# Performance work log

Hardware: AMD Instinct MI355X
Metric: run time of the kernel (lower is better)

## Reference

```python
import jax, jax.numpy as jnp
import numpy as np

HEADS = 8
HEAD_DIM = 64
SCALE = (2 * HEAD_DIM) ** -0.5


def setup_inputs() -> dict:
    key = jax.random.key(0)
    k1, k2, k3, k4, k5 = jax.random.split(key, 5)
    B, N, D = 2, 2048, 512
    inner = HEADS * HEAD_DIM  # 512
    return {
        "x1": jax.random.normal(k1, (B, N, D), dtype=jnp.float32),
        "x2": jax.random.normal(k2, (B, N, D), dtype=jnp.float32),
        "W_qkv1": jax.random.normal(k3, (D, 3 * inner), dtype=jnp.float32) * 0.02,
        "W_qkv2": jax.random.normal(k4, (D, 3 * inner), dtype=jnp.float32) * 0.02,
        "W_out": jax.random.normal(k5, (inner, D), dtype=jnp.float32) * 0.02,
        "b_out": jnp.zeros((D,), dtype=jnp.float32),
    }


def _split_heads(t):
    # [b, n, h*d] -> [b, h, n, d]
    b, n, hd = t.shape
    return t.reshape(b, n, HEADS, HEAD_DIM).transpose(0, 2, 1, 3)


def reference(x1, x2, W_qkv1, W_qkv2, W_out, b_out):
    qkv1 = x1 @ W_qkv1  # [b, n, 3*inner]
    qkv2 = x2 @ W_qkv2
    q1, k1, v1 = (_split_heads(t) for t in jnp.split(qkv1, 3, axis=-1))
    q2, k2, v2 = (_split_heads(t) for t in jnp.split(qkv2, 3, axis=-1))

    # fused dual-stream logits: scale * (q1 k1^T + q2 k2^T)  [b, h, n, n]
    dots = SCALE * (jnp.einsum("bhnd,bhmd->bhnm", q1, k1)
                    + jnp.einsum("bhnd,bhmd->bhnm", q2, k2))
    attn = jax.nn.softmax(dots, axis=-1)

    out1 = jnp.einsum("bhnm,bhmd->bhnd", attn, v1)
    out2 = jnp.einsum("bhnm,bhmd->bhnd", attn, v2)

    def _merge(t):
        b, h, n, d = t.shape
        return t.transpose(0, 2, 1, 3).reshape(b, n, h * d)

    out = jnp.concatenate([_merge(out1), _merge(out2)], axis=1)  # [b, 2n, inner]
    return out @ W_out + b_out
```

## Files before the change

### kernel.cpp

```cpp
#include <hip/hip_runtime.h>
#include <hip/hip_bf16.h>

typedef __attribute__((ext_vector_type(8))) short bf16x8;
typedef __attribute__((ext_vector_type(4))) float f32x4;
typedef __attribute__((ext_vector_type(16))) float f32x16;
typedef __attribute__((ext_vector_type(4))) short s16x4;
typedef __attribute__((ext_vector_type(4))) int i32x4;

#define MFMA(a, b, c) __builtin_amdgcn_mfma_f32_16x16x32_bf16(a, b, c, 0, 0, 0)
#define MFMA32(a, b, c) __builtin_amdgcn_mfma_f32_32x32x16_bf16(a, b, c, 0, 0, 0)

#define SCALE_F 0.08838834764831845f

__device__ __forceinline__ short f2bf(float f) {
  __hip_bfloat16 h = __float2bfloat16(f);
  return *reinterpret_cast<short*>(&h);
}

__device__ __forceinline__ void gld_lds16(const void* g, void* s) {
  __builtin_amdgcn_global_load_lds(
      (const __attribute__((address_space(1))) void*)g,
      (__attribute__((address_space(3))) void*)s, 16, 0, 0);
}

__global__ void cast_bf16_dual(const float* __restrict__ a,
                               const float* __restrict__ b,
                               short* __restrict__ oa, short* __restrict__ ob,
                               int n) {
  int idx = (blockIdx.x * 256 + threadIdx.x) * 4;
  const float* src = a;
  short* dst = oa;
  if (idx >= n) { idx -= n; src = b; dst = ob; }
  float4 v = *(const float4*)&src[idx];
  s16x4 o;
  o.x = f2bf(v.x); o.y = f2bf(v.y); o.z = f2bf(v.z); o.w = f2bf(v.w);
  *(s16x4*)&dst[idx] = o;
}

__global__ __launch_bounds__(256) void cast_transpose_tiled(
    const float* __restrict__ Wq1, const float* __restrict__ Wq2,
    const float* __restrict__ Wo, short* __restrict__ W1t,
    short* __restrict__ W2t, short* __restrict__ Wot) {
  __shared__ float t[64][65];
  int bid = blockIdx.x;
  const float* src;
  short* dst;
  int C, r0, c0;
  bool isq;
  if (bid < 384) {
    src = (bid < 192) ? Wq1 : Wq2;
    dst = (bid < 192) ? W1t : W2t;
    int tb = bid % 192;
    C = 1536; isq = true;
    r0 = (tb / 24) * 64; c0 = (tb % 24) * 64;
  } else {
    src = Wo; dst = Wot;
    int tb = bid - 384;
    C = 512; isq = false;
    r0 = (tb / 8) * 64; c0 = (tb % 8) * 64;
  }
  const int tid = threadIdx.x;
  const int lr = tid >> 4, lc = (tid & 15) * 4;
#pragma unroll
  for (int i = 0; i < 4; ++i) {
    float4 v = *(const float4*)&src[(size_t)(r0 + lr + 16 * i) * C + c0 + lc];
    t[lr + 16 * i][lc + 0] = v.x;
    t[lr + 16 * i][lc + 1] = v.y;
    t[lr + 16 * i][lc + 2] = v.z;
    t[lr + 16 * i][lc + 3] = v.w;
  }
  __syncthreads();
  const int oc = tid >> 2, orr = (tid & 3) * 16;
  const float sc = (isq && (c0 + oc) < 512) ? SCALE_F : 1.0f;
  short* dbase = dst + (size_t)(c0 + oc) * 512 + r0 + orr;
#pragma unroll
  for (int jj = 0; jj < 4; ++jj) {
    s16x4 ov;
    ov.x = f2bf(t[orr + 4 * jj + 0][oc] * sc);
    ov.y = f2bf(t[orr + 4 * jj + 1][oc] * sc);
    ov.z = f2bf(t[orr + 4 * jj + 2][oc] * sc);
    ov.w = f2bf(t[orr + 4 * jj + 3][oc] * sc);
    *(s16x4*)&dbase[4 * jj] = ov;
  }
}

__global__ __launch_bounds__(256) void gemm_qkv(
    const short* __restrict__ xb1, const short* __restrict__ xb2,
    const short* __restrict__ W1t, const short* __restrict__ W2t,
    short* __restrict__ QK1, short* __restrict__ QK2,
    short* __restrict__ Vt1, short* __restrict__ Vt2) {
  __shared__ short As[128 * 64];
  __shared__ short Bs[128 * 64];
  const int tid = threadIdx.x;
  const int w = tid >> 6, l = tid & 63;
  const int sid = blockIdx.y >= 12;
  const short* A = sid ? xb2 : xb1;
  const short* Bt = sid ? W2t : W1t;
  short* C0 = sid ? QK2 : QK1;
  short* C1 = sid ? Vt2 : Vt1;
  const int m0 = blockIdx.x * 128;
  const int n0 = (sid ? blockIdx.y - 12 : blockIdx.y) * 128;
  const int mi = (w >> 1) * 64, ni = (w & 1) * 64;
  const int lrow = l & 15, lk8 = (l >> 4) * 8;
  const int K = 512;

  f32x4 acc[4][4] = {};

  for (int k0 = 0; k0 < K; k0 += 64) {
    for (int g = 0; g < 4; ++g) {
      int c = g * 256 + w * 64 + l;
      int row = c >> 3, c8 = (c & 7) * 8;
      int ldsoff = (g * 256 + w * 64) * 8;
      gld_lds16(A + (size_t)(m0 + row) * K + k0 + c8, (void*)(As + ldsoff));
      gld_lds16(Bt + (size_t)(n0 + row) * K + k0 + c8, (void*)(Bs + ldsoff));
    }
    __syncthreads();
    __builtin_amdgcn_s_setprio(1);
    for (int kp = 0; kp < 2; ++kp) {
      bf16x8 af[4], bfr[4];
      for (int mf = 0; mf < 4; ++mf)
        af[mf] = *(const bf16x8*)&As[(mi + mf * 16 + lrow) * 64 + kp * 32 + lk8];
      for (int nf = 0; nf < 4; ++nf)
        bfr[nf] = *(const bf16x8*)&Bs[(ni + nf * 16 + lrow) * 64 + kp * 32 + lk8];
      for (int mf = 0; mf < 4; ++mf)
        for (int nf = 0; nf < 4; ++nf)
          acc[mf][nf] = MFMA(af[mf], bfr[nf], acc[mf][nf]);
    }
    __builtin_amdgcn_s_setprio(0);
    __syncthreads();
  }

  for (int mf = 0; mf < 4; ++mf)
    for (int nf = 0; nf < 4; ++nf)
      for (int r = 0; r < 4; ++r) {
        int row = m0 + mi + mf * 16 + (l >> 4) * 4 + r;
        int col = n0 + ni + nf * 16 + lrow;
        float v = acc[mf][nf][r];
        if (col < 1024) {
          C0[(size_t)row * 1024 + col] = f2bf(v);
        } else {
          int b = row >> 11, n = row & 2047;
          int cv = col - 1024, h = cv >> 6, d = cv & 63;
          C1[(((size_t)(b * 8 + h) * 64 + d) << 11) + n] = f2bf(v);
        }
      }
}

__global__ __launch_bounds__(256) void gemm_out(const short* __restrict__ A,
                                                const short* __restrict__ Bt,
                                                float* __restrict__ Cf,
                                                const float* __restrict__ bias) {
  __shared__ short As[64 * 64];
  __shared__ short Bs[128 * 64];
  const int tid = threadIdx.x;
  const int w = tid >> 6, l = tid & 63;
  const int m0 = blockIdx.x * 64, n0 = blockIdx.y * 128;
  const int mi = (w >> 1) * 32, ni = (w & 1) * 64;
  const int lrow = l & 15, lk8 = (l >> 4) * 8;
  const int K = 512, N = 512;

  f32x4 acc[2][4] = {};

  for (int k0 = 0; k0 < K; k0 += 64) {
    for (int g = 0; g < 2; ++g) {
      int c = g * 256 + tid;
      int row = c >> 3, c8 = (c & 7) * 8;
      gld_lds16(A + (size_t)(m0 + row) * K + k0 + c8, (void*)(As + c * 8));
    }
    for (int g = 0; g < 4; ++g) {
      int c = g * 256 + tid;
      int row = c >> 3, c8 = (c & 7) * 8;
      gld_lds16(Bt + (size_t)(n0 + row) * K + k0 + c8, (void*)(Bs + c * 8));
    }
    __syncthreads();
    __builtin_amdgcn_s_setprio(1);
    for (int kp = 0; kp < 2; ++kp) {
      bf16x8 af[2], bfr[4];
      for (int mf = 0; mf < 2; ++mf)
        af[mf] = *(const bf16x8*)&As[(mi + mf * 16 + lrow) * 64 + kp * 32 + lk8];
      for (int nf = 0; nf < 4; ++nf)
        bfr[nf] = *(const bf16x8*)&Bs[(ni + nf * 16 + lrow) * 64 + kp * 32 + lk8];
      for (int mf = 0; mf < 2; ++mf)
        for (int nf = 0; nf < 4; ++nf)
          acc[mf][nf] = MFMA(af[mf], bfr[nf], acc[mf][nf]);
    }
    __builtin_amdgcn_s_setprio(0);
    __syncthreads();
  }

  for (int mf = 0; mf < 2; ++mf)
    for (int nf = 0; nf < 4; ++nf)
      for (int r = 0; r < 4; ++r) {
        int row = m0 + mi + mf * 16 + (l >> 4) * 4 + r;
        int col = n0 + ni + nf * 16 + lrow;
        Cf[(size_t)row * N + col] = acc[mf][nf][r] + bias[col];
      }
}

__global__ __launch_bounds__(256, 2) void attn_kernel(
    const short* __restrict__ QK1, const short* __restrict__ QK2,
    const short* __restrict__ Vt1, const short* __restrict__ Vt2,
    short* __restrict__ Ocat) {
  __shared__ short lds[32768];
  short* K1s = lds;
  short* K2s = lds + 8192;
  short* V1s = lds + 16384;
  short* V2s = lds + 24576;

  const int tid = threadIdx.x;
  const int w = tid >> 6, l = tid & 63;
  const int wq = w & 1, wk = w >> 1;
  const int lq = l & 31, hi = l >> 5;
  const int qb = blockIdx.x, bh = blockIdx.y;
  const int b = bh >> 3, h = bh & 7;

  const short* Q1p = QK1 + (size_t)b * 2048 * 1024 + h * 64;
  const short* K1p = Q1p + 512;
  const short* Q2p = QK2 + (size_t)b * 2048 * 1024 + h * 64;
  const short* K2p = Q2p + 512;
  const short* V1p = Vt1 + (size_t)bh * 64 * 2048;
  const short* V2p = Vt2 + (size_t)bh * 64 * 2048;

  const int qrow = qb * 64 + wq * 32 + lq;
  bf16x8 q1f[4], q2f[4];
#pragma unroll
  for (int ck = 0; ck < 4; ++ck) {
    q1f[ck] = *(const bf16x8*)&Q1p[(size_t)qrow * 1024 + ck * 16 + hi * 8];
    q2f[ck] = *(const bf16x8*)&Q2p[(size_t)qrow * 1024 + ck * 16 + hi * 8];
  }

  f32x16 o1a = {}, o1b = {}, o2a = {}, o2b = {};
  float mrun = -1e30f, lrun = 0.f;

  auto stage_K = [&](int buf, int kt) {
    const int kv0 = kt * 64;
#pragma unroll
    for (int gg = 0; gg < 2; ++gg) {
      int cl = gg * 256 + tid;
      int row = cl >> 3;
      int lc = (cl & 7) ^ (row & 7);
      int lr = row & 31;
      int krow = kv0 + ((row >> 5) << 5) + (((lr >> 3) & 1) << 4) +
                 (((lr >> 2) & 1) << 3) + (((lr >> 4) & 1) << 2) + (lr & 3);
      int doff = buf * 4096 + cl * 8;
      gld_lds16(K1p + (size_t)krow * 1024 + lc * 8, (void*)(K1s + doff));
      gld_lds16(K2p + (size_t)krow * 1024 + lc * 8, (void*)(K2s + doff));
    }
  };
  auto stage_V = [&](int buf, int kt) {
    const int kv0 = kt * 64;
#pragma unroll
    for (int gg = 0; gg < 2; ++gg) {
      int cl = gg * 256 + tid;
      int row = cl >> 3;
      int lc = (cl & 7) ^ (row & 7);
      int doff = buf * 4096 + cl * 8;
      gld_lds16(V1p + (size_t)row * 2048 + kv0 + lc * 8, (void*)(V1s + doff));
      gld_lds16(V2p + (size_t)row * 2048 + kv0 + lc * 8, (void*)(V2s + doff));
    }
  };
  auto swo = [&](int row, int kc) { return row * 64 + ((kc ^ (row & 7)) * 8); };

  auto qk_tile = [&](int buf) -> f32x16 {
    const int krd = 32 * wk + lq;
    f32x16 s = {};
    __builtin_amdgcn_s_setprio(1);
#pragma unroll
    for (int ck = 0; ck < 4; ++ck) {
      bf16x8 k1 = *(const bf16x8*)&K1s[buf * 4096 + swo(krd, 2 * ck + hi)];
      bf16x8 k2 = *(const bf16x8*)&K2s[buf * 4096 + swo(krd, 2 * ck + hi)];
      s = MFMA32(k1, q1f[ck], s);
      s = MFMA32(k2, q2f[ck], s);
    }
    __builtin_amdgcn_s_setprio(0);
    return s;
  };

  auto smpv = [&](int buf, f32x16 s) {
    float mx = s[0];
#pragma unroll
    for (int i = 1; i < 16; ++i) mx = fmaxf(mx, s[i]);
    if (!__all(mx - mrun <= 8.0f)) {
      float rm = fmaxf(mx, __shfl_xor(mx, 32));
      float newm = fmaxf(mrun, rm);
      float corr = __expf(mrun - newm);
      mrun = newm;
      lrun *= corr;
#pragma unroll
      for (int i = 0; i < 16; ++i) {
        o1a[i] *= corr; o1b[i] *= corr; o2a[i] *= corr; o2b[i] *= corr;
      }
    }
    float p[16];
#pragma unroll
    for (int i = 0; i < 16; ++i) { p[i] = __expf(s[i] - mrun); lrun += p[i]; }

    __hip_bfloat162 a0 = __float22bfloat162_rn(float2{p[0], p[1]});
    __hip_bfloat162 a1 = __float22bfloat162_rn(float2{p[2], p[3]});
    __hip_bfloat162 a2 = __float22bfloat162_rn(float2{p[8], p[9]});
    __hip_bfloat162 a3 = __float22bfloat162_rn(float2{p[10], p[11]});
    __hip_bfloat162 b0 = __float22bfloat162_rn(float2{p[4], p[5]});
    __hip_bfloat162 b1 = __float22bfloat162_rn(float2{p[6], p[7]});
    __hip_bfloat162 b2 = __float22bfloat162_rn(float2{p[12], p[13]});
    __hip_bfloat162 b3 = __float22bfloat162_rn(float2{p[14], p[15]});
    i32x4 w0 = {*(int*)&a0, *(int*)&a1, *(int*)&a2, *(int*)&a3};
    i32x4 w1 = {*(int*)&b0, *(int*)&b1, *(int*)&b2, *(int*)&b3};
    bf16x8 pb0 = *(bf16x8*)&w0, pb1 = *(bf16x8*)&w1;

    __builtin_amdgcn_s_setprio(1);
#pragma unroll
    for (int c = 0; c < 2; ++c) {
      bf16x8 pb = c ? pb1 : pb0;
      int kcv = 4 * wk + 2 * c + hi;
      bf16x8 v1a = *(const bf16x8*)&V1s[buf * 4096 + swo(lq, kcv)];
      bf16x8 v1b = *(const bf16x8*)&V1s[buf * 4096 + swo(32 + lq, kcv)];
      bf16x8 v2a = *(const bf16x8*)&V2s[buf * 4096 + swo(lq, kcv)];
      bf16x8 v2b = *(const bf16x8*)&V2s[buf * 4096 + swo(32 + lq, kcv)];
      o1a = MFMA32(v1a, pb, o1a);
      o1b = MFMA32(v1b, pb, o1b);
      o2a = MFMA32(v2a, pb, o2a);
      o2b = MFMA32(v2b, pb, o2b);
    }
    __builtin_amdgcn_s_setprio(0);
  };

  stage_K(0, 0);
  stage_V(0, 0);
  stage_K(1, 1);
  asm volatile("s_waitcnt vmcnt(4)" ::: "memory");
  __builtin_amdgcn_s_barrier();
  f32x16 sprev = qk_tile(0);
  stage_V(1, 1);

  int cur = 0;
  for (int t = 0; t < 31; ++t) {
    asm volatile("s_waitcnt vmcnt(4) lgkmcnt(0)" ::: "memory");
    __builtin_amdgcn_s_barrier();
    if (t < 30) stage_K(cur, t + 2);
    f32x16 snew = qk_tile(cur ^ 1);
    smpv(cur, sprev);
    asm volatile("s_waitcnt lgkmcnt(0)" ::: "memory");
    __builtin_amdgcn_s_barrier();
    if (t < 30) stage_V(cur, t + 2);
    sprev = snew;
    cur ^= 1;
  }
  asm volatile("s_waitcnt vmcnt(0)" ::: "memory");
  __builtin_amdgcn_s_barrier();
  smpv(cur, sprev);

  lrun += __shfl_xor(lrun, 32);
  float* cb = (float*)lds;
  float* rg = cb + wq * 4224;
  if (wk == 1) {
#pragma unroll
    for (int i = 0; i < 16; ++i) {
      rg[i * 64 + l] = o1a[i];
      rg[(16 + i) * 64 + l] = o1b[i];
      rg[(32 + i) * 64 + l] = o2a[i];
      rg[(48 + i) * 64 + l] = o2b[i];
    }
    rg[4096 + l] = mrun;
    rg[4160 + l] = lrun;
  }
  __syncthreads();
  if (wk == 0) {
    float m1 = rg[4096 + l], l1 = rg[4160 + l];
    float mstar = fmaxf(mrun, m1);
    float e0 = __expf(mrun - mstar), e1 = __expf(m1 - mstar);
    float inv = 1.0f / (lrun * e0 + l1 * e1);
    float av0 = e0 * inv, av1 = e1 * inv;
#pragma unroll
    for (int i = 0; i < 16; ++i) {
      o1a[i] = o1a[i] * av0 + rg[i * 64 + l] * av1;
      o1b[i] = o1b[i] * av0 + rg[(16 + i) * 64 + l] * av1;
      o2a[i] = o2a[i] * av0 + rg[(32 + i) * 64 + l] * av1;
      o2b[i] = o2b[i] * av0 + rg[(48 + i) * 64 + l] * av1;
    }
    const size_t base1 = ((size_t)b * 4096 + qrow) * 512 + h * 64;
    const size_t base2 = base1 + (size_t)2048 * 512;
#pragma unroll
    for (int rq = 0; rq < 4; ++rq) {
      int d0 = 8 * rq + 4 * hi;
      s16x4 ov;
      ov.x = f2bf(o1a[rq * 4 + 0]); ov.y = f2bf(o1a[rq * 4 + 1]);
      ov.z = f2bf(o1a[rq * 4 + 2]); ov.w = f2bf(o1a[rq * 4 + 3]);
      *(s16x4*)&Ocat[base1 + d0] = ov;
      ov.x = f2bf(o1b[rq * 4 + 0]); ov.y = f2bf(o1b[rq * 4 + 1]);
      ov.z = f2bf(o1b[rq * 4 + 2]); ov.w = f2bf(o1b[rq * 4 + 3]);
      *(s16x4*)&Ocat[base1 + 32 + d0] = ov;
      ov.x = f2bf(o2a[rq * 4 + 0]); ov.y = f2bf(o2a[rq * 4 + 1]);
      ov.z = f2bf(o2a[rq * 4 + 2]); ov.w = f2bf(o2a[rq * 4 + 3]);
      *(s16x4*)&Ocat[base2 + d0] = ov;
      ov.x = f2bf(o2b[rq * 4 + 0]); ov.y = f2bf(o2b[rq * 4 + 1]);
      ov.z = f2bf(o2b[rq * 4 + 2]); ov.w = f2bf(o2b[rq * 4 + 3]);
      *(s16x4*)&Ocat[base2 + 32 + d0] = ov;
    }
  }
}

extern "C" void kernel_launch(void* const* d_in, const int* in_sizes, int n_in,
                              void* d_out, int out_size, void* d_ws,
                              size_t ws_size, hipStream_t stream) {
  const float* x1 = (const float*)d_in[0];
  const float* x2 = (const float*)d_in[1];
  const float* Wq1 = (const float*)d_in[2];
  const float* Wq2 = (const float*)d_in[3];
  const float* Wo = (const float*)d_in[4];
  const float* bo = (const float*)d_in[5];
  float* out = (float*)d_out;

  short* p = (short*)d_ws;
  short* xb1 = p;  p += (size_t)4096 * 512;
  short* xb2 = p;  p += (size_t)4096 * 512;
  short* W1t = p;  p += (size_t)1536 * 512;
  short* W2t = p;  p += (size_t)1536 * 512;
  short* Wot = p;  p += (size_t)512 * 512;
  short* QK1 = p;  p += (size_t)4096 * 1024;
  short* QK2 = p;  p += (size_t)4096 * 1024;
  short* Vt1 = p;  p += (size_t)2 * 8 * 64 * 2048;
  short* Vt2 = p;  p += (size_t)2 * 8 * 64 * 2048;
  short* Ocat = p; p += (size_t)8192 * 512;

  cast_bf16_dual<<<4096, 256, 0, stream>>>(x1, x2, xb1, xb2, 4096 * 512);
  cast_transpose_tiled<<<448, 256, 0, stream>>>(Wq1, Wq2, Wo, W1t, W2t, Wot);

  gemm_qkv<<<dim3(32, 24), 256, 0, stream>>>(xb1, xb2, W1t, W2t, QK1, QK2,
                                             Vt1, Vt2);

  attn_kernel<<<dim3(32, 16), 256, 0, stream>>>(QK1, QK2, Vt1, Vt2, Ocat);

  gemm_out<<<dim3(128, 4), 256, 0, stream>>>(Ocat, Wot, out, bo);
}
```

Baseline: 102.3 us.

## Merge cast kernels, use exp2 softmax, simplify attention pipeline to single-stage prefetch

Merges the input-cast and weight cast-transpose kernels into one launch to save a kernel launch. Folds log2(e) into the Q scaling so softmax uses exp2 directly, removing a multiply per exponential. Replaces the software-pipelined attention loop (QK of the next tile overlapped with softmax/PV of the previous, K and V staged separately) with a simpler double-buffered loop that prefetches K and V together for the next tile. The simpler schedule loses the cross-tile overlap of the QK MFMAs with the softmax work.

```diff
diff --git a/kernel.cpp b/kernel.cpp
--- a/kernel.cpp
+++ b/kernel.cpp
@@ -11,6 +11,9 @@
 #define MFMA32(a, b, c) __builtin_amdgcn_mfma_f32_32x32x16_bf16(a, b, c, 0, 0, 0)
 
 #define SCALE_F 0.08838834764831845f
+#define LOG2E_F 1.4426950408889634f
+#define THR2 11.541560327111708f
+#define EXP2(x) __builtin_exp2f(x)
 
 __device__ __forceinline__ short f2bf(float f) {
   __hip_bfloat16 h = __float2bfloat16(f);
@@ -23,26 +26,27 @@
       (__attribute__((address_space(3))) void*)s, 16, 0, 0);
 }
 
-__global__ void cast_bf16_dual(const float* __restrict__ a,
-                               const float* __restrict__ b,
-                               short* __restrict__ oa, short* __restrict__ ob,
-                               int n) {
-  int idx = (blockIdx.x * 256 + threadIdx.x) * 4;
-  const float* src = a;
-  short* dst = oa;
-  if (idx >= n) { idx -= n; src = b; dst = ob; }
-  float4 v = *(const float4*)&src[idx];
-  s16x4 o;
-  o.x = f2bf(v.x); o.y = f2bf(v.y); o.z = f2bf(v.z); o.w = f2bf(v.w);
-  *(s16x4*)&dst[idx] = o;
-}
-
-__global__ __launch_bounds__(256) void cast_transpose_tiled(
+__global__ __launch_bounds__(256) void preprocess(
+    const float* __restrict__ x1, const float* __restrict__ x2,
     const float* __restrict__ Wq1, const float* __restrict__ Wq2,
-    const float* __restrict__ Wo, short* __restrict__ W1t,
-    short* __restrict__ W2t, short* __restrict__ Wot) {
+    const float* __restrict__ Wo, short* __restrict__ xb1,
+    short* __restrict__ xb2, short* __restrict__ W1t, short* __restrict__ W2t,
+    short* __restrict__ Wot) {
   __shared__ float t[64][65];
+  const int tid = threadIdx.x;
   int bid = blockIdx.x;
+  if (bid < 4096) {
+    int idx = (bid * 256 + tid) * 4;
+    const float* src = x1;
+    short* dst = xb1;
+    if (idx >= 4096 * 512) { idx -= 4096 * 512; src = x2; dst = xb2; }
+    float4 v = *(const float4*)&src[idx];
+    s16x4 o;
+    o.x = f2bf(v.x); o.y = f2bf(v.y); o.z = f2bf(v.z); o.w = f2bf(v.w);
+    *(s16x4*)&dst[idx] = o;
+    return;
+  }
+  bid -= 4096;
   const float* src;
   short* dst;
   int C, r0, c0;
@@ -59,7 +63,6 @@
     C = 512; isq = false;
     r0 = (tb / 8) * 64; c0 = (tb % 8) * 64;
   }
-  const int tid = threadIdx.x;
   const int lr = tid >> 4, lc = (tid & 15) * 4;
 #pragma unroll
   for (int i = 0; i < 4; ++i) {
@@ -71,7 +74,8 @@
   }
   __syncthreads();
   const int oc = tid >> 2, orr = (tid & 3) * 16;
-  const float sc = (isq && (c0 + oc) < 512) ? SCALE_F : 1.0f;
+  const float sc =
+      (isq && (c0 + oc) < 512) ? SCALE_F * LOG2E_F : 1.0f;
   short* dbase = dst + (size_t)(c0 + oc) * 512 + r0 + orr;
 #pragma unroll
   for (int jj = 0; jj < 4; ++jj) {
@@ -232,7 +236,7 @@
   f32x16 o1a = {}, o1b = {}, o2a = {}, o2b = {};
   float mrun = -1e30f, lrun = 0.f;
 
-  auto stage_K = [&](int buf, int kt) {
+  auto stage = [&](int buf, int kt) {
     const int kv0 = kt * 64;
 #pragma unroll
     for (int gg = 0; gg < 2; ++gg) {
@@ -245,45 +249,43 @@
       int doff = buf * 4096 + cl * 8;
       gld_lds16(K1p + (size_t)krow * 1024 + lc * 8, (void*)(K1s + doff));
       gld_lds16(K2p + (size_t)krow * 1024 + lc * 8, (void*)(K2s + doff));
-    }
-  };
-  auto stage_V = [&](int buf, int kt) {
-    const int kv0 = kt * 64;
-#pragma unroll
-    for (int gg = 0; gg < 2; ++gg) {
-      int cl = gg * 256 + tid;
-      int row = cl >> 3;
-      int lc = (cl & 7) ^ (row & 7);
-      int doff = buf * 4096 + cl * 8;
       gld_lds16(V1p + (size_t)row * 2048 + kv0 + lc * 8, (void*)(V1s + doff));
       gld_lds16(V2p + (size_t)row * 2048 + kv0 + lc * 8, (void*)(V2s + doff));
     }
   };
   auto swo = [&](int row, int kc) { return row * 64 + ((kc ^ (row & 7)) * 8); };
 
-  auto qk_tile = [&](int buf) -> f32x16 {
+  int cur = 0;
+  stage(0, 0);
+
+  for (int kt = 0; kt < 32; ++kt) {
+    if (kt + 1 < 32) {
+      stage(cur ^ 1, kt + 1);
+      asm volatile("s_waitcnt vmcnt(8)" ::: "memory");
+    } else {
+      asm volatile("s_waitcnt vmcnt(0)" ::: "memory");
+    }
+    __builtin_amdgcn_s_barrier();
+
     const int krd = 32 * wk + lq;
     f32x16 s = {};
     __builtin_amdgcn_s_setprio(1);
 #pragma unroll
     for (int ck = 0; ck < 4; ++ck) {
-      bf16x8 k1 = *(const bf16x8*)&K1s[buf * 4096 + swo(krd, 2 * ck + hi)];
-      bf16x8 k2 = *(const bf16x8*)&K2s[buf * 4096 + swo(krd, 2 * ck + hi)];
+      bf16x8 k1 = *(const bf16x8*)&K1s[cur * 4096 + swo(krd, 2 * ck + hi)];
+      bf16x8 k2 = *(const bf16x8*)&K2s[cur * 4096 + swo(krd, 2 * ck + hi)];
       s = MFMA32(k1, q1f[ck], s);
       s = MFMA32(k2, q2f[ck], s);
     }
     __builtin_amdgcn_s_setprio(0);
-    return s;
-  };
-
-  auto smpv = [&](int buf, f32x16 s) {
+
     float mx = s[0];
 #pragma unroll
     for (int i = 1; i < 16; ++i) mx = fmaxf(mx, s[i]);
-    if (!__all(mx - mrun <= 8.0f)) {
+    if (!__all(mx - mrun <= THR2)) {
       float rm = fmaxf(mx, __shfl_xor(mx, 32));
       float newm = fmaxf(mrun, rm);
-      float corr = __expf(mrun - newm);
+      float corr = EXP2(mrun - newm);
       mrun = newm;
       lrun *= corr;
 #pragma unroll
@@ -293,7 +295,7 @@
     }
     float p[16];
 #pragma unroll
-    for (int i = 0; i < 16; ++i) { p[i] = __expf(s[i] - mrun); lrun += p[i]; }
+    for (int i = 0; i < 16; ++i) { p[i] = EXP2(s[i] - mrun); lrun += p[i]; }
 
     __hip_bfloat162 a0 = __float22bfloat162_rn(float2{p[0], p[1]});
     __hip_bfloat162 a1 = __float22bfloat162_rn(float2{p[2], p[3]});
@@ -312,42 +314,21 @@
     for (int c = 0; c < 2; ++c) {
       bf16x8 pb = c ? pb1 : pb0;
       int kcv = 4 * wk + 2 * c + hi;
-      bf16x8 v1a = *(const bf16x8*)&V1s[buf * 4096 + swo(lq, kcv)];
-      bf16x8 v1b = *(const bf16x8*)&V1s[buf * 4096 + swo(32 + lq, kcv)];
-      bf16x8 v2a = *(const bf16x8*)&V2s[buf * 4096 + swo(lq, kcv)];
-      bf16x8 v2b = *(const bf16x8*)&V2s[buf * 4096 + swo(32 + lq, kcv)];
+      bf16x8 v1a = *(const bf16x8*)&V1s[cur * 4096 + swo(lq, kcv)];
+      bf16x8 v1b = *(const bf16x8*)&V1s[cur * 4096 + swo(32 + lq, kcv)];
+      bf16x8 v2a = *(const bf16x8*)&V2s[cur * 4096 + swo(lq, kcv)];
+      bf16x8 v2b = *(const bf16x8*)&V2s[cur * 4096 + swo(32 + lq, kcv)];
       o1a = MFMA32(v1a, pb, o1a);
       o1b = MFMA32(v1b, pb, o1b);
       o2a = MFMA32(v2a, pb, o2a);
       o2b = MFMA32(v2b, pb, o2b);
     }
     __builtin_amdgcn_s_setprio(0);
-  };
-
-  stage_K(0, 0);
-  stage_V(0, 0);
-  stage_K(1, 1);
-  asm volatile("s_waitcnt vmcnt(4)" ::: "memory");
-  __builtin_amdgcn_s_barrier();
-  f32x16 sprev = qk_tile(0);
-  stage_V(1, 1);
-
-  int cur = 0;
-  for (int t = 0; t < 31; ++t) {
-    asm volatile("s_waitcnt vmcnt(4) lgkmcnt(0)" ::: "memory");
-    __builtin_amdgcn_s_barrier();
-    if (t < 30) stage_K(cur, t + 2);
-    f32x16 snew = qk_tile(cur ^ 1);
-    smpv(cur, sprev);
+
     asm volatile("s_waitcnt lgkmcnt(0)" ::: "memory");
     __builtin_amdgcn_s_barrier();
-    if (t < 30) stage_V(cur, t + 2);
-    sprev = snew;
     cur ^= 1;
   }
-  asm volatile("s_waitcnt vmcnt(0)" ::: "memory");
-  __builtin_amdgcn_s_barrier();
-  smpv(cur, sprev);
 
   lrun += __shfl_xor(lrun, 32);
   float* cb = (float*)lds;
@@ -367,7 +348,7 @@
   if (wk == 0) {
     float m1 = rg[4096 + l], l1 = rg[4160 + l];
     float mstar = fmaxf(mrun, m1);
-    float e0 = __expf(mrun - mstar), e1 = __expf(m1 - mstar);
+    float e0 = EXP2(mrun - mstar), e1 = EXP2(m1 - mstar);
     float inv = 1.0f / (lrun * e0 + l1 * e1);
     float av0 = e0 * inv, av1 = e1 * inv;
 #pragma unroll
@@ -422,8 +403,8 @@
   short* Vt2 = p;  p += (size_t)2 * 8 * 64 * 2048;
   short* Ocat = p; p += (size_t)8192 * 512;
 
-  cast_bf16_dual<<<4096, 256, 0, stream>>>(x1, x2, xb1, xb2, 4096 * 512);
-  cast_transpose_tiled<<<448, 256, 0, stream>>>(Wq1, Wq2, Wo, W1t, W2t, Wot);
+  preprocess<<<4544, 256, 0, stream>>>(x1, x2, Wq1, Wq2, Wo, xb1, xb2, W1t,
+                                       W2t, Wot);
 
   gemm_qkv<<<dim3(32, 24), 256, 0, stream>>>(xb1, xb2, W1t, W2t, QK1, QK2,
                                              Vt1, Vt2);
```

Measured after the change: 104.7 us. 1.02x slower.
